# Kernel tuning notes

Measured on AMD Instinct MI355X. Metric: run time of the kernel, lower is better.

## Reference

```python
import jax, jax.numpy as jnp
import numpy as np

M, N, B, T = 512, 2048, 8192, 5
P, P_MAX = 0.012, 0.12


def setup_inputs() -> dict:
    key = jax.random.key(0)
    k1, k2 = jax.random.split(key)
    A = jax.random.normal(k1, (M, N), dtype=jnp.float32) / np.float32(np.sqrt(M))
    y = jax.random.normal(k2, (B, M), dtype=jnp.float32)
    # norm = 1.001 * ||A^T A||_2 (largest singular value), as in __init__
    norm = np.float32(1.001 * np.linalg.norm(np.asarray(A).T @ np.asarray(A), 2))
    beta = jnp.ones((T + 1, 1, 1), jnp.float32) * (np.float32(0.1) / norm)
    mu = jnp.ones((T + 1, 1, 1), jnp.float32) / norm
    W = A.T  # Linear weight overwritten with A.T; W(y) = y @ W.T = y @ A
    return {"y": y, "A": A, "W": W, "beta": beta, "mu": mu}


def _shrink(x, beta, t):
    # top-p hard-threshold with softshrink fallback
    abs_x = jnp.abs(x)
    idx = int(min(P * t, P_MAX) * x.shape[-1])  # static per unrolled step
    if idx > 0:
        thr = jax.lax.top_k(abs_x, idx)[0][:, idx - 1:idx]  # [B,1] p-th largest |x|
    else:
        thr = jnp.zeros((x.shape[0], 1), x.dtype)
    u = x / beta
    x_soft = beta * (jnp.sign(u) * jnp.maximum(jnp.abs(u) - 1.0, 0.0))  # beta*softshrink(x/beta,1)
    return jnp.where(abs_x >= thr, x, x_soft)


def reference(y, A, W, beta, mu):
    # W(v) = v @ W.T ; W initialized to A.T so W(y) = y @ A
    h = mu[0] * (y @ W.T)            # [B, N]
    x = _shrink(h, beta[0], 0)
    for t in range(1, T + 1):
        r = x @ A.T - y              # [B, M] residual
        k = mu[t] * (r @ W.T)        # [B, N]
        x = _shrink(x - k, beta[t], t)
    return x
```

## Files before the change

kernel.cpp:

```cpp
#include <hip/hip_runtime.h>


typedef int int4v __attribute__((ext_vector_type(4)));

__device__ __forceinline__ void quant2(float v, float inv_s,
                                       signed char& q1, signed char& q0) {
    int q = __float2int_rn(v * inv_s);
    q = q > 16256 ? 16256 : (q < -16256 ? -16256 : q);
    int hi = (q + 64) >> 7;
    q1 = (signed char)hi;
    q0 = (signed char)(q - (hi << 7));
}

__device__ __forceinline__ void gl_lds16(const signed char* g, signed char* lds) {
    __builtin_amdgcn_global_load_lds(
        (const __attribute__((address_space(1))) void*)g,
        (__attribute__((address_space(3))) void*)lds, 16, 0, 0);
}

template<int BN, int WM, int WN, int EPI>
__global__ __launch_bounds__(WM * WN * 64, (WM * WN == 8) ? 4 : 2)
void gemm_i8(
    const signed char* __restrict__ A1, const signed char* __restrict__ A0, int lda,
    const signed char* __restrict__ B1, const signed char* __restrict__ B0, int ldb,
    const float* __restrict__ sAv,
    const float* __restrict__ sBv,
    const float* __restrict__ Yaux,
    const float* __restrict__ Zprev,
    const float* __restrict__ thrv,
    const float* __restrict__ bPrev,
    float* __restrict__ outF,
    const float* __restrict__ muPtr, int muIdx, int K, int ldOut)
{
    constexpr int NTHR = WM * WN * 64;
    constexpr int MI   = 128 / WM / 16;
    constexpr int NJf  = BN / WN / 16;
    constexpr int AR   = 512 / NTHR;
    constexpr int BR   = (BN * 4) / NTHR;
    constexpr int LPT  = 2 * (AR + BR);
    constexpr int ASZ  = 128 * 64;
    constexpr int BSZ  = BN * 64;

    __shared__ signed char smem[4 * ASZ + 4 * BSZ];
    signed char* const As1p = smem;
    signed char* const As0p = smem + 2 * ASZ;
    signed char* const Bs1p = smem + 4 * ASZ;
    signed char* const Bs0p = smem + 4 * ASZ + 2 * BSZ;

    const int tid  = threadIdx.x;
    const int wid  = tid >> 6;
    const int lane = tid & 63;
    const int quad = lane >> 4;
    const int l16  = lane & 15;
    const int waveM = (wid / WN) * (MI * 16);
    const int waveN = (wid % WN) * (NJf * 16);
    const int swz   = (l16 >> 1) & 3;

    const int flat  = blockIdx.x + gridDim.x * blockIdx.y;
    const int mBase = (flat & 63) * 128;
    const int nBase = (flat >> 6) * BN;

    int4v accH[MI][NJf] = {};
    int4v accM[MI][NJf] = {};

    auto stage = [&](int b, int k0) {
        #pragma unroll
        for (int rr = 0; rr < AR; ++rr) {
            int c   = rr * NTHR + tid;
            int row = c >> 2;
            int js  = (c & 3) ^ ((row >> 1) & 3);
            size_t ga = (size_t)(mBase + row) * lda + k0 + js * 16;
            size_t doff = (size_t)(b * ASZ + (rr * NTHR + wid * 64) * 16);
            gl_lds16(A1 + ga, As1p + doff);
            gl_lds16(A0 + ga, As0p + doff);
        }
        #pragma unroll
        for (int rr = 0; rr < BR; ++rr) {
            int c   = rr * NTHR + tid;
            int row = c >> 2;
            int js  = (c & 3) ^ ((row >> 1) & 3);
            size_t gb = (size_t)(nBase + row) * ldb + k0 + js * 16;
            size_t doff = (size_t)(b * BSZ + (rr * NTHR + wid * 64) * 16);
            gl_lds16(B1 + gb, Bs1p + doff);
            gl_lds16(B0 + gb, Bs0p + doff);
        }
    };

    const int KT = K >> 6;
    stage(0, 0);

    for (int kt = 0; kt < KT; ++kt) {
        const int cur = kt & 1;
        if (kt + 1 < KT) {
            stage(cur ^ 1, (kt + 1) << 6);
            if constexpr (LPT == 4)      asm volatile("s_waitcnt vmcnt(4)" ::: "memory");
            else if constexpr (LPT == 6) asm volatile("s_waitcnt vmcnt(6)" ::: "memory");
            else                         asm volatile("s_waitcnt vmcnt(8)" ::: "memory");
        } else {
            asm volatile("s_waitcnt vmcnt(0)" ::: "memory");
        }
        __builtin_amdgcn_s_barrier();

        int4v a1[MI], a0[MI], b1[NJf], b0[NJf];
        #pragma unroll
        for (int i = 0; i < MI; ++i) {
            int off = (waveM + i * 16 + l16) * 64 + ((quad ^ swz) * 16);
            a1[i] = *(const int4v*)(As1p + cur * ASZ + off);
            a0[i] = *(const int4v*)(As0p + cur * ASZ + off);
        }
        #pragma unroll
        for (int j = 0; j < NJf; ++j) {
            int off = (waveN + j * 16 + l16) * 64 + ((quad ^ swz) * 16);
            b1[j] = *(const int4v*)(Bs1p + cur * BSZ + off);
            b0[j] = *(const int4v*)(Bs0p + cur * BSZ + off);
        }
        __builtin_amdgcn_s_setprio(1);
        #pragma unroll
        for (int i = 0; i < MI; ++i)
            #pragma unroll
            for (int j = 0; j < NJf; ++j) {
                accH[i][j] = __builtin_amdgcn_mfma_i32_16x16x64_i8(a1[i], b1[j], accH[i][j], 0, 0, 0);
                accM[i][j] = __builtin_amdgcn_mfma_i32_16x16x64_i8(a1[i], b0[j], accM[i][j], 0, 0, 0);
                accM[i][j] = __builtin_amdgcn_mfma_i32_16x16x64_i8(a0[i], b1[j], accM[i][j], 0, 0, 0);
            }
        __builtin_amdgcn_s_setprio(0);
        __builtin_amdgcn_s_barrier();
    }

    const float mu = muPtr[muIdx];
    const float betaPrev = (EPI == 2) ? bPrev[0] : 0.f;
    float* const epi = (float*)smem;

    #pragma unroll
    for (int i = 0; i < MI; ++i) {
        #pragma unroll
        for (int j = 0; j < NJf; ++j) {
            const int lr0 = waveM + i * 16 + quad * 4;
            const int lc  = waveN + j * 16 + l16;
            const float sB = sBv[nBase + lc];
            #pragma unroll
            for (int r2 = 0; r2 < 4; ++r2) {
                const int lr = lr0 + r2;
                const float sA = sAv[mBase + lr];
                epi[lr * BN + lc] = sA * sB *
                    ((float)accH[i][j][r2] * 16384.f
                   + (float)accM[i][j][r2] * 128.f);
            }
        }
    }
    __syncthreads();

    constexpr int C4   = BN / 4;
    constexpr int PASS = (128 * C4) / NTHR;
    #pragma unroll
    for (int p = 0; p < PASS; ++p) {
        const int e  = p * NTHR + tid;
        const int lr = e / C4;
        const int c4 = e % C4;
        const int gr = mBase + lr;
        const size_t idx = (size_t)gr * ldOut + nBase + c4 * 4;
        const float4 v4 = *(const float4*)&epi[lr * BN + c4 * 4];
        float4 o;
        if constexpr (EPI == 0) {
            o.x = mu * v4.x; o.y = mu * v4.y;
            o.z = mu * v4.z; o.w = mu * v4.w;
        } else if constexpr (EPI == 1) {
            const float4 ya = *(const float4*)&Yaux[idx];
            o.x = v4.x - ya.x; o.y = v4.y - ya.y;
            o.z = v4.z - ya.z; o.w = v4.w - ya.w;
        } else {
            const float4 zp = *(const float4*)&Zprev[idx];
            const unsigned tb = __float_as_uint(thrv[gr]);
            const float zc[4] = {zp.x, zp.y, zp.z, zp.w};
            const float vc[4] = {v4.x, v4.y, v4.z, v4.w};
            float oc[4];
            #pragma unroll
            for (int k4 = 0; k4 < 4; ++k4) {
                const unsigned ab = __float_as_uint(fabsf(zc[k4]));
                float xv;
                if (ab >= tb) {
                    xv = zc[k4];
                } else {
                    xv = copysignf(
                        fmaxf(__uint_as_float(ab) - betaPrev, 0.f), zc[k4]);
                }
                oc[k4] = xv - mu * vc[k4];
            }
            o.x = oc[0]; o.y = oc[1]; o.z = oc[2]; o.w = oc[3];
        }
        *(float4*)&outF[idx] = o;
    }
}

template<int COLS>
__global__ __launch_bounds__(256) void rowquant_kernel(
    const float* __restrict__ src,
    signed char* __restrict__ q1, signed char* __restrict__ q0,
    float* __restrict__ scale)
{
    const int wid  = threadIdx.x >> 6;
    const int lane = threadIdx.x & 63;
    const long long row = (long long)blockIdx.x * 4 + wid;
    constexpr int EP = COLS / 256;
    const float* s = src + row * COLS;

    float v[EP * 4];
    #pragma unroll
    for (int c = 0; c < EP; ++c) {
        float4 f = ((const float4*)s)[c * 64 + lane];
        v[c * 4 + 0] = f.x; v[c * 4 + 1] = f.y; v[c * 4 + 2] = f.z; v[c * 4 + 3] = f.w;
    }
    float mx = 0.f;
    #pragma unroll
    for (int i = 0; i < EP * 4; ++i) mx = fmaxf(mx, fabsf(v[i]));
    #pragma unroll
    for (int off = 32; off >= 1; off >>= 1) mx = fmaxf(mx, __shfl_xor(mx, off, 64));
    mx = fmaxf(mx, 1e-20f);
    if (lane == 0) scale[row] = mx / 16256.f;
    const float inv = 16256.f / mx;

    #pragma unroll
    for (int c = 0; c < EP; ++c) {
        size_t col = (size_t)(c * 64 + lane) * 4;
        signed char h[4], l[4];
        #pragma unroll
        for (int e = 0; e < 4; ++e) quant2(v[c * 4 + e], inv, h[e], l[e]);
        *(char4*)(q1 + row * COLS + col) = *(char4*)h;
        *(char4*)(q0 + row * COLS + col) = *(char4*)l;
    }
}

__global__ __launch_bounds__(256) void shrink_kernel(
    float* __restrict__ z,
    signed char* __restrict__ X1, signed char* __restrict__ X0,
    float* __restrict__ sX, float* __restrict__ thrOut,
    const float* __restrict__ betaPtr, int tIdx, int kSel,
    int writeF32, int writePlanes)
{
    const int wid  = threadIdx.x >> 6;
    const int lane = threadIdx.x & 63;
    const long long row = (long long)blockIdx.x * 4 + wid;
    float* zr = z + row * 2048;

    float v[32];
    #pragma unroll
    for (int c = 0; c < 8; ++c) {
        float4 f = ((const float4*)zr)[c * 64 + lane];
        v[c * 4 + 0] = f.x; v[c * 4 + 1] = f.y; v[c * 4 + 2] = f.z; v[c * 4 + 3] = f.w;
    }

    if (kSel > 0) {
        const float beta = betaPtr[tIdx];
        unsigned a[32];
        #pragma unroll
        for (int i = 0; i < 32; ++i) a[i] = __float_as_uint(fabsf(v[i]));

        unsigned lo = 0u, hi = 0x7F800000u;
        #pragma unroll 1
        for (int it = 0; it < 31; ++it) {
            const unsigned mid = (lo + hi) >> 1;
            int cnt = 0;
            #pragma unroll
            for (int i = 0; i < 32; ++i)
                cnt += (int)__popcll(__ballot(a[i] >= mid));
            if (cnt >= kSel) {
                lo = mid;
                if (cnt == kSel) break;
            } else {
                hi = mid;
            }
        }
        const unsigned thr = lo;
        if (lane == 0) thrOut[row] = __uint_as_float(thr);
        #pragma unroll
        for (int i = 0; i < 32; ++i) {
            if (a[i] < thr) {
                float av   = __uint_as_float(a[i]);
                float soft = fmaxf(av - beta, 0.f);
                v[i] = copysignf(soft, v[i]);
            }
        }
    } else {
        if (lane == 0) thrOut[row] = 0.f;
    }

    float mx = 0.f;
    #pragma unroll
    for (int i = 0; i < 32; ++i) mx = fmaxf(mx, fabsf(v[i]));
    #pragma unroll
    for (int off = 32; off >= 1; off >>= 1) mx = fmaxf(mx, __shfl_xor(mx, off, 64));
    mx = fmaxf(mx, 1e-20f);
    if (writePlanes && lane == 0) sX[row] = mx / 16256.f;
    const float inv = 16256.f / mx;

    #pragma unroll
    for (int c = 0; c < 8; ++c) {
        size_t col = (size_t)(c * 64 + lane) * 4;
        if (writePlanes) {
            signed char h[4], l[4];
            #pragma unroll
            for (int e = 0; e < 4; ++e) quant2(v[c * 4 + e], inv, h[e], l[e]);
            *(char4*)(X1 + row * 2048 + col) = *(char4*)h;
            *(char4*)(X0 + row * 2048 + col) = *(char4*)l;
        }
        if (writeF32) {
            float4 f;
            f.x = v[c * 4 + 0]; f.y = v[c * 4 + 1]; f.z = v[c * 4 + 2]; f.w = v[c * 4 + 3];
            ((float4*)zr)[c * 64 + lane] = f;
        }
    }
}

extern "C" void kernel_launch(void* const* d_in, const int* in_sizes, int n_in,
                              void* d_out, int out_size, void* d_ws, size_t ws_size,
                              hipStream_t stream)
{
    const float* y    = (const float*)d_in[0];
    const float* A    = (const float*)d_in[1];
    const float* W    = (const float*)d_in[2];
    const float* beta = (const float*)d_in[3];
    const float* mu   = (const float*)d_in[4];
    float* out = (float*)d_out;

    signed char* A1q  = (signed char*)d_ws;
    signed char* A0q  = A1q  + 512 * 2048;
    signed char* AT1q = A0q  + 512 * 2048;
    signed char* AT0q = AT1q + 2048 * 512;
    signed char* y1q  = AT0q + 2048 * 512;
    signed char* y0q  = y1q  + 8192 * 512;
    signed char* x1q  = y0q  + 8192 * 512;
    signed char* x0q  = x1q  + (size_t)8192 * 2048;
    signed char* r1q  = x0q  + (size_t)8192 * 2048;
    signed char* r0q  = r1q  + 8192 * 512;
    float* rF  = (float*)(r0q + 8192 * 512);
    float* sa  = rF + (size_t)8192 * 512;
    float* sat = sa  + 512;
    float* sy  = sat + 2048;
    float* sx  = sy  + 8192;
    float* sr  = sx  + 8192;
    float* thr = sr  + 8192;

    rowquant_kernel<2048><<<128, 256, 0, stream>>>(A, A1q, A0q, sa);
    rowquant_kernel<512><<<512, 256, 0, stream>>>(W, AT1q, AT0q, sat);
    rowquant_kernel<512><<<2048, 256, 0, stream>>>(y, y1q, y0q, sy);

    gemm_i8<128, 4, 2, 0><<<dim3(16, 64), 512, 0, stream>>>(
        y1q, y0q, 512, AT1q, AT0q, 512, sy, sat,
        nullptr, nullptr, nullptr, nullptr, out, mu, 0, 512, 2048);
    shrink_kernel<<<2048, 256, 0, stream>>>(out, x1q, x0q, sx, thr, beta,
                                            0, 0, 0, 1);

    for (int t = 1; t <= 5; ++t) {
        double p = 0.012 * t; if (p > 0.12) p = 0.12;
        int kSel = (int)(p * 2048.0);

        gemm_i8<64, 2, 2, 1><<<dim3(8, 64), 256, 0, stream>>>(
            x1q, x0q, 2048, A1q, A0q, 2048, sx, sa,
            y, nullptr, nullptr, nullptr, rF, mu, t, 2048, 512);
        rowquant_kernel<512><<<2048, 256, 0, stream>>>(rF, r1q, r0q, sr);

        gemm_i8<128, 4, 2, 2><<<dim3(16, 64), 512, 0, stream>>>(
            r1q, r0q, 512, AT1q, AT0q, 512, sr, sat,
            nullptr, out, thr, beta + (t - 1), out, mu, t, 512, 2048);

        shrink_kernel<<<2048, 256, 0, stream>>>(out, x1q, x0q, sx, thr, beta,
                                                t, kSel, t == 5 ? 1 : 0,
                                                t < 5 ? 1 : 0);
    }
}
```

Measured before the change: 701.4 us.

## Use 8-wave blocks for residual GEMM and XCD-aware row remap in row kernels

The residual GEMM (x·Aᵀ) moves from 4 waves to 8 waves per block. Because the B tile is now smaller than one load round, only some waves load B, and the per-wave vmcnt waits are split to match. The row-wise quant and shrink kernels remap block indices so that consecutive blocks on the same XCD touch neighbouring rows, aiming for better L2 locality with the GEMM tiling. The waits differ per wave and the remap adds index arithmetic, so a miscounted wait would be a correctness risk.

```diff
diff --git a/kernel.cpp b/kernel.cpp
--- a/kernel.cpp
+++ b/kernel.cpp
@@ -16,6 +16,14 @@
     __builtin_amdgcn_global_load_lds(
         (const __attribute__((address_space(1))) void*)g,
         (__attribute__((address_space(3))) void*)lds, 16, 0, 0);
+}
+
+__device__ __forceinline__ long long xcd_row(int b, int wid, int remap) {
+    if (remap) {
+        const int m = (b & 7) + 8 * (b >> 8);
+        return (long long)m * 128 + (((b >> 3) & 31) << 2) + wid;
+    }
+    return (long long)b * 4 + wid;
 }
 
 template<int BN, int WM, int WN, int EPI>
@@ -35,11 +43,12 @@
     constexpr int NTHR = WM * WN * 64;
     constexpr int MI   = 128 / WM / 16;
     constexpr int NJf  = BN / WN / 16;
-    constexpr int AR   = 512 / NTHR;
-    constexpr int BR   = (BN * 4) / NTHR;
-    constexpr int LPT  = 2 * (AR + BR);
+    constexpr int ACH  = 512;
+    constexpr int BCH  = BN * 4;
+    constexpr bool BSPLIT = (BCH < NTHR);
     constexpr int ASZ  = 128 * 64;
     constexpr int BSZ  = BN * 64;
+    constexpr int LPT_ALL = 2 * (ACH / NTHR) + (BSPLIT ? 0 : 2 * (BCH / NTHR));
 
     __shared__ signed char smem[4 * ASZ + 4 * BSZ];
     signed char* const As1p = smem;
@@ -65,7 +74,7 @@
 
     auto stage = [&](int b, int k0) {
         #pragma unroll
-        for (int rr = 0; rr < AR; ++rr) {
+        for (int rr = 0; rr < ACH / NTHR; ++rr) {
             int c   = rr * NTHR + tid;
             int row = c >> 2;
             int js  = (c & 3) ^ ((row >> 1) & 3);
@@ -74,15 +83,27 @@
             gl_lds16(A1 + ga, As1p + doff);
             gl_lds16(A0 + ga, As0p + doff);
         }
-        #pragma unroll
-        for (int rr = 0; rr < BR; ++rr) {
-            int c   = rr * NTHR + tid;
-            int row = c >> 2;
-            int js  = (c & 3) ^ ((row >> 1) & 3);
-            size_t gb = (size_t)(nBase + row) * ldb + k0 + js * 16;
-            size_t doff = (size_t)(b * BSZ + (rr * NTHR + wid * 64) * 16);
-            gl_lds16(B1 + gb, Bs1p + doff);
-            gl_lds16(B0 + gb, Bs0p + doff);
+        if constexpr (!BSPLIT) {
+            #pragma unroll
+            for (int rr = 0; rr < BCH / NTHR; ++rr) {
+                int c   = rr * NTHR + tid;
+                int row = c >> 2;
+                int js  = (c & 3) ^ ((row >> 1) & 3);
+                size_t gb = (size_t)(nBase + row) * ldb + k0 + js * 16;
+                size_t doff = (size_t)(b * BSZ + (rr * NTHR + wid * 64) * 16);
+                gl_lds16(B1 + gb, Bs1p + doff);
+                gl_lds16(B0 + gb, Bs0p + doff);
+            }
+        } else {
+            if (wid < BCH / 64) {
+                int c   = tid;
+                int row = c >> 2;
+                int js  = (c & 3) ^ ((row >> 1) & 3);
+                size_t gb = (size_t)(nBase + row) * ldb + k0 + js * 16;
+                size_t doff = (size_t)(b * BSZ + wid * 64 * 16);
+                gl_lds16(B1 + gb, Bs1p + doff);
+                gl_lds16(B0 + gb, Bs0p + doff);
+            }
         }
     };
 
@@ -93,9 +114,14 @@
         const int cur = kt & 1;
         if (kt + 1 < KT) {
             stage(cur ^ 1, (kt + 1) << 6);
-            if constexpr (LPT == 4)      asm volatile("s_waitcnt vmcnt(4)" ::: "memory");
-            else if constexpr (LPT == 6) asm volatile("s_waitcnt vmcnt(6)" ::: "memory");
-            else                         asm volatile("s_waitcnt vmcnt(8)" ::: "memory");
+            if constexpr (BSPLIT) {
+                if (wid < BCH / 64) asm volatile("s_waitcnt vmcnt(4)" ::: "memory");
+                else                asm volatile("s_waitcnt vmcnt(2)" ::: "memory");
+            } else if constexpr (LPT_ALL == 4) {
+                asm volatile("s_waitcnt vmcnt(4)" ::: "memory");
+            } else {
+                asm volatile("s_waitcnt vmcnt(6)" ::: "memory");
+            }
         } else {
             asm volatile("s_waitcnt vmcnt(0)" ::: "memory");
         }
@@ -196,11 +222,11 @@
 __global__ __launch_bounds__(256) void rowquant_kernel(
     const float* __restrict__ src,
     signed char* __restrict__ q1, signed char* __restrict__ q0,
-    float* __restrict__ scale)
+    float* __restrict__ scale, int remap8k)
 {
     const int wid  = threadIdx.x >> 6;
     const int lane = threadIdx.x & 63;
-    const long long row = (long long)blockIdx.x * 4 + wid;
+    const long long row = xcd_row(blockIdx.x, wid, remap8k);
     constexpr int EP = COLS / 256;
     const float* s = src + row * COLS;
 
@@ -239,7 +265,7 @@
 {
     const int wid  = threadIdx.x >> 6;
     const int lane = threadIdx.x & 63;
-    const long long row = (long long)blockIdx.x * 4 + wid;
+    const long long row = xcd_row(blockIdx.x, wid, 1);
     float* zr = z + row * 2048;
 
     float v[32];
@@ -340,9 +366,9 @@
     float* sr  = sx  + 8192;
     float* thr = sr  + 8192;
 
-    rowquant_kernel<2048><<<128, 256, 0, stream>>>(A, A1q, A0q, sa);
-    rowquant_kernel<512><<<512, 256, 0, stream>>>(W, AT1q, AT0q, sat);
-    rowquant_kernel<512><<<2048, 256, 0, stream>>>(y, y1q, y0q, sy);
+    rowquant_kernel<2048><<<128, 256, 0, stream>>>(A, A1q, A0q, sa, 0);
+    rowquant_kernel<512><<<512, 256, 0, stream>>>(W, AT1q, AT0q, sat, 0);
+    rowquant_kernel<512><<<2048, 256, 0, stream>>>(y, y1q, y0q, sy, 1);
 
     gemm_i8<128, 4, 2, 0><<<dim3(16, 64), 512, 0, stream>>>(
         y1q, y0q, 512, AT1q, AT0q, 512, sy, sat,
@@ -354,10 +380,10 @@
         double p = 0.012 * t; if (p > 0.12) p = 0.12;
         int kSel = (int)(p * 2048.0);
 
-        gemm_i8<64, 2, 2, 1><<<dim3(8, 64), 256, 0, stream>>>(
+        gemm_i8<64, 4, 2, 1><<<dim3(8, 64), 512, 0, stream>>>(
             x1q, x0q, 2048, A1q, A0q, 2048, sx, sa,
             y, nullptr, nullptr, nullptr, rF, mu, t, 2048, 512);
-        rowquant_kernel<512><<<2048, 256, 0, stream>>>(rF, r1q, r0q, sr);
+        rowquant_kernel<512><<<2048, 256, 0, stream>>>(rF, r1q, r0q, sr, 1);
 
         gemm_i8<128, 4, 2, 2><<<dim3(16, 64), 512, 0, stream>>>(
             r1q, r0q, 512, AT1q, AT0q, 512, sr, sat,
```

Measured after the change: 725.7 us. +3.5%, slower.
